# Optimization experiments

Hardware: AMD Instinct MI355X
Metric: run time of the kernel (lower is better)

The kernel has to match this reference:

```python
import jax, jax.numpy as jnp
import numpy as np
import math

CHUNK = 32
NS_STEPS = 5
MAX_GNORM = 10.0


def _normalize(x, eps=1e-12):
    n = jnp.linalg.norm(x, axis=-1, keepdims=True)
    return x / jnp.maximum(n, eps)


def _poly(x):  # poly_degree = 2: [x, x^2] / sqrt(2)
    return jnp.concatenate([x, x * x], axis=-1) / math.sqrt(2.0)


def _ns5(G):
    # Muon-style Newton-Schulz orthogonalization (quintic, 5 steps)
    a, b, c = 3.4445, -4.7750, 2.0315
    t = G.shape[0] > G.shape[1]
    X = G.T if t else G
    X = X / (jnp.linalg.norm(X) + 1e-7)
    for _ in range(NS_STEPS):
        A = X @ X.T
        B = b * A + c * (A @ A)
        X = a * X + B @ X
    return X.T if t else X


def _clip_mean(g):
    # per-sample grad-norm clipping to MAX_GNORM, then mean over samples
    n = g.shape[0]
    norms = jnp.maximum(jnp.linalg.norm(g.reshape(n, -1), axis=1), 1e-8)
    scale = jnp.maximum(norms / MAX_GNORM, 1.0)
    return jnp.mean(g / scale.reshape((n,) + (1,) * (g.ndim - 1)), axis=0)


def _mem_fwd(W0, W1, z):  # MemoryMLP depth=2, gelu (exact) between layers
    return jax.nn.gelu(z @ W0, approximate=False) @ W1


def setup_inputs() -> dict:
    key = jax.random.key(0)
    ks = jax.random.split(key, 16)
    B, S, D, M, P, H = 2, 1024, 2048, 512, 1024, 2048
    w = lambda k, shape, fan_in: jax.random.normal(k, shape, jnp.float32) / np.float32(np.sqrt(fan_in))
    return {
        "x": jax.random.normal(ks[0], (B, S, D), jnp.float32),
        "Wk": w(ks[1], (M, D), D),
        "Wv": w(ks[2], (M, D), D),
        "Wq": w(ks[3], (M, D), D),
        "Wout": w(ks[4], (D, M), M),
        "w_lr": w(ks[5], (1, D), D), "b_lr": jnp.full((1,), -4.0, jnp.float32),
        "w_mom": w(ks[6], (1, D), D), "b_mom": jnp.full((1,), 1.0, jnp.float32),
        "w_dec": w(ks[7], (1, D), D), "b_dec": jnp.full((1,), -3.0, jnp.float32),
        "w_gate": w(ks[8], (1, D), D), "b_gate": jnp.full((1,), -1.0, jnp.float32),
        "Wmem0": w(ks[9], (P, H), P),
        "Wmem1": w(ks[10], (H, P), H),
        "Wmemout": w(ks[11], (P, M), P),
        "Wvexp": w(ks[12], (M, P), M),
    }


def reference(x, Wk, Wv, Wq, Wout, w_lr, b_lr, w_mom, b_mom, w_dec, b_dec,
              w_gate, b_gate, Wmem0, Wmem1, Wmemout, Wvexp):
    # Inference path (torch.is_grad_enabled() == False): chunked ATLAS update.
    B, S, D = x.shape
    NC = S // CHUNK

    k = _normalize(x @ Wk.T)          # (B,S,M)
    v = x @ Wv.T                       # (B,S,M)
    q = _normalize(x @ Wq.T)          # (B,S,M)
    kp = _poly(k)                      # (B,S,P)
    qp = _poly(q)                      # (B,S,P)
    vexp = v @ Wvexp                   # v_expand: (B,S,P)

    gate = lambda w, b: jax.nn.sigmoid(jnp.einsum('bsd,od->bso', x, w) + b)
    lr, mom, dec, og = gate(w_lr, b_lr), gate(w_mom, b_mom), gate(w_dec, b_dec), gate(w_gate, b_gate)

    cmean = lambda t: t[..., 0].reshape(B, NC, CHUNK).mean(axis=(0, 2))  # per-chunk scalar
    lr_c, mom_c, dec_c = cmean(lr), cmean(mom), cmean(dec)

    chunks = lambda t: t.reshape(B, NC, CHUNK, t.shape[-1]).transpose(1, 0, 2, 3)  # (NC,B,C,F)
    qc, kc, vc = chunks(qp), chunks(kp), chunks(vexp)

    def loss_fn(params, kk, vv):  # ||M(k) - v||^2 per sample
        W0_, W1_ = params
        pred = jax.nn.gelu(kk @ W0_, approximate=False) @ W1_
        return jnp.sum((pred - vv) ** 2)

    grad_fn = jax.vmap(jax.grad(loss_fn), in_axes=((None, None), 0, 0))

    def step(carry, xs):
        W0, W1, S0, S1 = carry
        qch, kch, vch, lrc, momc, decc = xs
        retr = _mem_fwd(W0, W1, qch) @ Wmemout  # retrieve with pre-update params: (B,C,M)
        kf = kch.reshape(-1, kch.shape[-1])
        vf = vch.reshape(-1, vch.shape[-1])
        g0, g1 = grad_fn((W0, W1), kf, vf)      # per-sample grads
        g0, g1 = _clip_mean(g0), _clip_mean(g1)
        s0 = momc * S0 - lrc * g0                # surprise momentum
        s1 = momc * S1 - lrc * g1
        W0n = (1.0 - decc) * W0 + _ns5(s0) * lrc # forget gate + orthogonalized step
        W1n = (1.0 - decc) * W1 + _ns5(s1) * lrc
        return (W0n, W1n, s0, s1), retr

    init = (Wmem0, Wmem1, jnp.zeros_like(Wmem0), jnp.zeros_like(Wmem1))
    _, retrs = jax.lax.scan(step, init, (qc, kc, vc, lr_c, mom_c, dec_c))
    retrieved = retrs.transpose(1, 0, 2, 3).reshape(B, S, -1)  # (B,S,M)
    delta = retrieved @ Wout.T
    return x + delta * og
```

## Files before the change

### kernel.cpp

```cpp
#include <hip/hip_runtime.h>


typedef unsigned short us;
typedef __attribute__((ext_vector_type(8))) short s16x8;
typedef __attribute__((ext_vector_type(8))) unsigned short u16x8;
typedef __attribute__((ext_vector_type(4))) float f32x4;

#define MKP 72

__device__ __forceinline__ float gelu_f(float x) {
  return 0.5f * x * (1.0f + erff(x * 0.70710678118654752f));
}
__device__ __forceinline__ float gelu_grad_f(float x) {
  float cdf = 0.5f * (1.0f + erff(x * 0.70710678118654752f));
  float pdf = 0.3989422804014327f * expf(-0.5f * x * x);
  return cdf + x * pdf;
}
__device__ __forceinline__ float sigmoid_f(float x) { return 1.0f / (1.0f + expf(-x)); }

__device__ __forceinline__ us f2bf(float f) {
  union { float f; unsigned u; } v; v.f = f;
  unsigned r = (v.u + 0x7FFFu + ((v.u >> 16) & 1u)) >> 16;
  return (us)r;
}
__device__ __forceinline__ float bf2f(us h) {
  union { unsigned u; float f; } v; v.u = ((unsigned)h) << 16;
  return v.f;
}
__device__ __forceinline__ int cm_map(int n) {
  return ((n & 1023) >> 5) * 64 + (n >> 10) * 32 + (n & 31);
}
__device__ __forceinline__ size_t pf_off(int r, int k, int KB) {
  return ((size_t)(r >> 4) * KB + (k >> 5)) * 512 + ((k >> 3) & 3) * 128 + (r & 15) * 8 + (k & 7);
}

__device__ __forceinline__ float block_reduce_sum(float v, float* red) {
  int t = threadIdx.x;
  red[t] = v; __syncthreads();
  for (int s = blockDim.x >> 1; s > 0; s >>= 1) {
    if (t < s) red[t] += red[t + s];
    __syncthreads();
  }
  float r = red[0];
  __syncthreads();
  return r;
}

__device__ __forceinline__ void gemm_pk(const us* __restrict__ A,
                                        const us* __restrict__ B, int KB,
                                        int lane, int m0, int n0,
                                        f32x4 (&acc)[4][4]) {
  const us* am[4];
  const us* bm[4];
#pragma unroll
  for (int q = 0; q < 4; ++q) {
    am[q] = A + (size_t)((m0 >> 4) + q) * KB * 512 + lane * 8;
    bm[q] = B + (size_t)((n0 >> 4) + q) * KB * 512 + lane * 8;
  }
#pragma unroll
  for (int i = 0; i < 4; ++i)
#pragma unroll
    for (int j = 0; j < 4; ++j) acc[i][j] = (f32x4){0.f, 0.f, 0.f, 0.f};
  u16x8 a0[4], b0[4], a1[4], b1[4];
#pragma unroll
  for (int q = 0; q < 4; ++q) {
    a0[q] = *(const u16x8*)(am[q]);
    b0[q] = *(const u16x8*)(bm[q]);
    a1[q] = *(const u16x8*)(am[q] + 512);
    b1[q] = *(const u16x8*)(bm[q] + 512);
  }
  for (int kb = 0; kb < KB; kb += 2) {
#pragma unroll
    for (int mi = 0; mi < 4; ++mi)
#pragma unroll
      for (int ni = 0; ni < 4; ++ni)
        acc[mi][ni] = __builtin_amdgcn_mfma_f32_16x16x32_bf16(
            (s16x8)a0[mi], (s16x8)b0[ni], acc[mi][ni], 0, 0, 0);
    if (kb + 2 < KB) {
#pragma unroll
      for (int q = 0; q < 4; ++q) {
        a0[q] = *(const u16x8*)(am[q] + (size_t)(kb + 2) * 512);
        b0[q] = *(const u16x8*)(bm[q] + (size_t)(kb + 2) * 512);
      }
    }
#pragma unroll
    for (int mi = 0; mi < 4; ++mi)
#pragma unroll
      for (int ni = 0; ni < 4; ++ni)
        acc[mi][ni] = __builtin_amdgcn_mfma_f32_16x16x32_bf16(
            (s16x8)a1[mi], (s16x8)b1[ni], acc[mi][ni], 0, 0, 0);
    if (kb + 3 < KB) {
#pragma unroll
      for (int q = 0; q < 4; ++q) {
        a1[q] = *(const u16x8*)(am[q] + (size_t)(kb + 3) * 512);
        b1[q] = *(const u16x8*)(bm[q] + (size_t)(kb + 3) * 512);
      }
    }
  }
}

template<int EPI, int TM, int TN>
__global__ __launch_bounds__(256)
void mgp_k(const us* __restrict__ Aq, const us* __restrict__ Bq,
           us* __restrict__ Cq, us* __restrict__ C2q, const us* __restrict__ Eq,
           int K, int N, float c1, float c2,
           long sA, long sB, long sC, long sE) {
  __shared__ __align__(16) us ct[4 * 64 * 72];
  const int tid = threadIdx.x;
  const int wave = tid >> 6, lane = tid & 63;
  const int l15 = lane & 15, l4 = lane >> 4;
  const int wm = (wave >> 1) * 64, wn = (wave & 1) * 64;
  const int TPB = TM * TN;
  const int t = blockIdx.x;
  const int bz = t / TPB;
  const int ti = t - bz * TPB;
  const int m0 = (ti / TN) * 128 + wm;
  const int n0 = (ti % TN) * 128 + wn;

  const us* A = Aq + (size_t)bz * sA;
  const us* B = Bq + (size_t)bz * sB;
  us* C = Cq + (size_t)bz * sC;
  us* C2 = C2q + (size_t)bz * sC;
  const us* E = Eq + (size_t)bz * sE;
  const int KB = K >> 5;

  f32x4 acc[4][4];
  gemm_pk(A, B, KB, lane, m0, n0, acc);

  us* cw = ct + wave * 64 * 72;
#pragma unroll
  for (int mi = 0; mi < 4; ++mi)
#pragma unroll
    for (int i = 0; i < 4; ++i)
#pragma unroll
      for (int ni = 0; ni < 4; ++ni)
        cw[(mi * 16 + l4 * 4 + i) * 72 + ni * 16 + l15] = f2bf(acc[mi][ni][i]);

  if constexpr (EPI == 20 || EPI == 21) {
    const int KC = N >> 5;
#pragma unroll
    for (int q = 0; q < 8; ++q) {
      u16x8 v = *(const u16x8*)&cw[lane * 72 + q * 8];
      size_t off = pf_off(m0 + lane, n0 + q * 8, KC);
      if constexpr (EPI == 21) {
        u16x8 e = *(const u16x8*)(E + off);
        u16x8 o;
#pragma unroll
        for (int w = 0; w < 8; ++w) o[w] = f2bf(c1 * bf2f(v[w]) + c2 * bf2f(e[w]));
        *(u16x8*)(C + off) = o;
      } else {
        *(u16x8*)(C + off) = v;
      }
    }
  } else if constexpr (EPI == 23) {
#pragma unroll
    for (int q = 0; q < 8; ++q) {
      size_t off = pf_off(m0 + lane, n0 + q * 8, 64);
      u16x8 v = *(const u16x8*)&cw[lane * 72 + q * 8];
      u16x8 e = *(const u16x8*)(E + off);
      u16x8 o;
#pragma unroll
      for (int w = 0; w < 8; ++w) o[w] = f2bf(bf2f(v[w]) + c1 * bf2f(e[w]));
      *(u16x8*)&cw[lane * 72 + q * 8] = o;
      *(u16x8*)(C + off) = o;
    }
#pragma unroll
    for (int q = 0; q < 8; ++q) {
      u16x8 o;
#pragma unroll
      for (int w = 0; w < 8; ++w) o[w] = cw[(q * 8 + w) * 72 + lane];
      size_t offT = pf_off(n0 + lane, m0 + q * 8, 32);
      *(u16x8*)(C2 + offT) = o;
    }
  } else {
#pragma unroll
    for (int q = 0; q < 8; ++q) {
      size_t off = pf_off(m0 + lane, n0 + q * 8, 64);
      u16x8 v = *(const u16x8*)&cw[lane * 72 + q * 8];
      u16x8 e = *(const u16x8*)(E + off);
      u16x8 o;
#pragma unroll
      for (int w = 0; w < 8; ++w) o[w] = f2bf(bf2f(v[w]) + c1 * bf2f(e[w]));
      *(u16x8*)(C + (size_t)(m0 + lane) * 2048 + n0 + q * 8) = o;
    }
  }
}

template<int EPI, int TM, int TN>
static void mgp(hipStream_t st, const us* A, const us* B, us* C, us* C2,
                const us* E, int K, int N, float c1, float c2,
                long sA, long sB, long sC, long sE) {
  dim3 g(TM * TN * 2), b(256);
  hipLaunchKernelGGL((mgp_k<EPI, TM, TN>), g, b, 0, st, A, B, C, C2, E,
                     K, N, c1, c2, sA, sB, sC, sE);
}

template<int EPI>
__device__ __forceinline__ float epilogue(f32x4 (&acc)[4][4], int m0, int n0,
    int l15, int l4, void* Cq, void* C2, const void* Eq,
    const float* FX, const float* OG, const float* cp, int cidx,
    int ldc, int lde, float c1, float c2) {
  float ssq = 0.f;
#pragma unroll
  for (int mi = 0; mi < 4; ++mi) {
#pragma unroll
    for (int i = 0; i < 4; ++i) {
      int grow = m0 + mi * 16 + l4 * 4 + i;
#pragma unroll
      for (int ni = 0; ni < 4; ++ni) {
        int col = n0 + ni * 16 + l15;
        float v = acc[mi][ni][i];
        if constexpr (EPI == 5) {
          ((us*)Cq)[(size_t)grow * ldc + col] = f2bf(v);
        } else if constexpr (EPI == 7) {
          ((float*)Cq)[(size_t)grow * ldc + col] = v;
        } else if constexpr (EPI == 8) {
          ((us*)Cq)[(size_t)grow * ldc + col] = f2bf(gelu_f(v));
          if (m0 >= 64)
            ((float*)C2)[(size_t)(grow - 64) * ldc + col] = gelu_grad_f(v);
        } else if constexpr (EPI == 9) {
          if (m0 < 64)
            ((us*)Cq)[(size_t)grow * ldc + col] = f2bf(v);
          else
            ((us*)Cq)[(size_t)grow * ldc + col] =
                f2bf(2.0f * (v - ((const float*)Eq)[(size_t)(grow - 64) * lde + col]));
        } else if constexpr (EPI == 13) {
          ((float*)Cq)[(size_t)grow * ldc + col] =
              v * ((const float*)Eq)[(size_t)grow * lde + col];
        } else if constexpr (EPI == 14) {
          float* C = (float*)Cq;
          float old = C[(size_t)grow * ldc + col];
          float nv = cp[cidx * 3 + 1] * old - cp[cidx * 3 + 0] * v;
          C[(size_t)grow * ldc + col] = nv;
          ssq += nv * nv;
        } else if constexpr (EPI == 15) {
          ((float*)Cq)[(size_t)grow * ldc + col] =
              FX[(size_t)grow * ldc + col] + v * OG[grow];
        } else if constexpr (EPI == 17) {
          int crow = cm_map(grow);
          ((float*)Cq)[(size_t)crow * ldc + col] = v;
        }
      }
    }
  }
  return ssq;
}

template<int EPI, int TA, int DUAL, int AG>
__device__ __forceinline__ float mg_body(const us* __restrict__ A0,
    const us* __restrict__ A2, const us* __restrict__ B,
    void* __restrict__ Cq, void* __restrict__ C2, const void* __restrict__ Eq,
    const float* __restrict__ FX, const float* __restrict__ OG,
    const float* __restrict__ cp, int cidx, int m0, int n0,
    int K, int lda, int ldb, int ldc, int lde, float c1, float c2,
    us* As, us* Bs, int t) {
  const us* A = A0;
  if constexpr (DUAL) { if (m0 >= 64) A = A2; }
  const int mA0 = DUAL ? (m0 & 63) : m0;
  const int l15 = t & 15, l4 = t >> 4;

  f32x4 acc[4][4];
#pragma unroll
  for (int i = 0; i < 4; ++i)
#pragma unroll
    for (int j = 0; j < 4; ++j) acc[i][j] = (f32x4){0.f, 0.f, 0.f, 0.f};

  const int srw = t >> 3;
  const int sck = (t & 7) * 8;

  u16x8 ra[8], rb[8];
  auto LDA = [&](int k0) {
#pragma unroll
    for (int p = 0; p < 8; ++p) {
      if constexpr (TA == 0) {
        int row = srw + p * 8;
        int srow;
        if constexpr (AG) srow = cm_map(m0 + row); else srow = mA0 + row;
        ra[p] = *(const u16x8*)(A + (size_t)srow * lda + k0 + sck);
      } else {
        ra[p] = *(const u16x8*)(A + (size_t)(k0 + srw + p * 8) * lda + mA0 + sck);
      }
    }
  };
  auto LDB = [&](int k0) {
#pragma unroll
    for (int p = 0; p < 8; ++p)
      rb[p] = *(const u16x8*)(B + (size_t)(n0 + srw + p * 8) * ldb + k0 + sck);
  };

  LDA(0); LDB(0);
  for (int k0 = 0; k0 < K; k0 += 64) {
    if constexpr (TA == 0) {
#pragma unroll
      for (int p = 0; p < 8; ++p)
        *(u16x8*)&As[(srw + p * 8) * MKP + sck] = ra[p];
    } else {
#pragma unroll
      for (int p = 0; p < 8; ++p) {
        int kk = srw + p * 8;
#pragma unroll
        for (int j = 0; j < 8; ++j) As[(sck + j) * MKP + kk] = ra[p][j];
      }
    }
#pragma unroll
    for (int p = 0; p < 8; ++p)
      *(u16x8*)&Bs[(srw + p * 8) * MKP + sck] = rb[p];
    if (k0 + 64 < K) { LDA(k0 + 64); LDB(k0 + 64); }
#pragma unroll
    for (int ks = 0; ks < 2; ++ks) {
      s16x8 af[4], bf[4];
#pragma unroll
      for (int mi = 0; mi < 4; ++mi)
        af[mi] = *(const s16x8*)&As[(mi * 16 + l15) * MKP + ks * 32 + l4 * 8];
#pragma unroll
      for (int ni = 0; ni < 4; ++ni)
        bf[ni] = *(const s16x8*)&Bs[(ni * 16 + l15) * MKP + ks * 32 + l4 * 8];
#pragma unroll
      for (int mi = 0; mi < 4; ++mi)
#pragma unroll
        for (int ni = 0; ni < 4; ++ni)
          acc[mi][ni] = __builtin_amdgcn_mfma_f32_16x16x32_bf16(af[mi], bf[ni], acc[mi][ni], 0, 0, 0);
    }
  }

  return epilogue<EPI>(acc, m0, n0, l15, l4, Cq, C2, Eq, FX, OG, cp, cidx,
                       ldc, lde, c1, c2);
}

template<int EPI, int TA, int DUAL, int AG>
__global__ __launch_bounds__(64)
void mg_k(const us* __restrict__ Aq, const us* __restrict__ A2,
          const us* __restrict__ Bq, void* __restrict__ Cq,
          void* __restrict__ C2, const void* __restrict__ Eq,
          const float* __restrict__ FX, const float* __restrict__ OG,
          const float* __restrict__ cp, int cidx,
          int M, int N, int K, int lda, int ldb, int ldc, int lde,
          float c1, float c2) {
  __shared__ __align__(16) us As[64 * MKP];
  __shared__ __align__(16) us Bs[64 * MKP];
  mg_body<EPI, TA, DUAL, AG>(Aq, A2, Bq, Cq, C2, Eq, FX, OG, cp, cidx,
                             blockIdx.y * 64, blockIdx.x * 64, K, lda, ldb,
                             ldc, lde, c1, c2, As, Bs, threadIdx.x);
}

template<int EPI, int TA = 0, int DUAL = 0, int AG = 0>
static void mg(hipStream_t st, const us* A, const us* A2, const us* B,
               void* C, void* C2, const void* E,
               const float* FX, const float* OG, const float* cp, int cidx,
               int M, int N, int K, int lda, int ldb, int ldc, int lde,
               float c1 = 0.f, float c2 = 0.f) {
  dim3 g(N / 64, M / 64, 1), b(64);
  hipLaunchKernelGGL((mg_k<EPI, TA, DUAL, AG>), g, b, 0, st, A, A2, B, C, C2, E,
                     FX, OG, cp, cidx, M, N, K, lda, ldb, ldc, lde, c1, c2);
}

__global__ __launch_bounds__(64)
void mg2_k(const us* __restrict__ kp_c, const us* __restrict__ dhT,
           float* __restrict__ S0, const us* __restrict__ habk,
           const us* __restrict__ rbwT, float* __restrict__ S1,
           const float* __restrict__ cp, int c, float* __restrict__ parts2) {
  __shared__ __align__(16) us As[64 * MKP];
  __shared__ __align__(16) us Bs[64 * MKP];
  int bid = blockIdx.x;
  float ssq;
  if (bid < 512) {
    int m0 = (bid >> 5) * 64, n0 = (bid & 31) * 64;
    ssq = mg_body<14, 1, 0, 0>(kp_c, nullptr, dhT, S0, nullptr, nullptr,
                               nullptr, nullptr, cp, c, m0, n0,
                               64, 1024, 64, 2048, 0, 0.f, 0.f, As, Bs, threadIdx.x);
  } else {
    int b2 = bid - 512;
    int m0 = (b2 >> 4) * 64, n0 = (b2 & 15) * 64;
    ssq = mg_body<14, 1, 0, 0>(habk, nullptr, rbwT, S1, nullptr, nullptr,
                               nullptr, nullptr, cp, c, m0, n0,
                               64, 2048, 64, 1024, 0, 0.f, 0.f, As, Bs, threadIdx.x);
  }
  for (int off = 32; off > 0; off >>= 1) ssq += __shfl_down(ssq, off);
  if (threadIdx.x == 0) parts2[bid] = ssq;
}

__global__ __launch_bounds__(64)
void mg34_k(const us* __restrict__ pr, const us* __restrict__ WmoT,
            us* __restrict__ retrv_c, const us* __restrict__ W1b,
            float* __restrict__ dh, const float* __restrict__ gp) {
  __shared__ __align__(16) us As[64 * MKP];
  __shared__ __align__(16) us Bs[64 * MKP];
  int bid = blockIdx.x;
  if (bid < 8) {
    mg_body<5, 0, 0, 0>(pr, nullptr, WmoT, retrv_c, nullptr, nullptr,
                        nullptr, nullptr, nullptr, 0, 0, bid * 64,
                        1024, 1024, 1024, 512, 0, 0.f, 0.f, As, Bs, threadIdx.x);
  } else {
    int b2 = bid - 8;
    mg_body<13, 0, 0, 0>(pr + 64 * 1024, nullptr, W1b, dh, nullptr, gp,
                         nullptr, nullptr, nullptr, 0, 0, b2 * 64,
                         1024, 1024, 1024, 2048, 2048, 0.f, 0.f, As, Bs, threadIdx.x);
  }
}

__global__ void wt2_k(const float* __restrict__ dh, const float* __restrict__ w0inv,
                      us* __restrict__ dhT, const us* __restrict__ prg,
                      const float* __restrict__ w1inv, us* __restrict__ rbwT) {
  __shared__ float tile[32][33];
  int bid = blockIdx.x;
  int tx = threadIdx.x, ty = threadIdx.y;
  int c0, r0, ldin;
  const float* wv;
  us* outp;
  bool f32in;
  const void* in;
  if (bid < 128) {
    in = dh; wv = w0inv; outp = dhT; ldin = 2048; f32in = true;
    c0 = (bid & 63) * 32; r0 = (bid >> 6) * 32;
  } else {
    int b2 = bid - 128;
    in = prg; wv = w1inv; outp = rbwT; ldin = 1024; f32in = false;
    c0 = (b2 & 31) * 32; r0 = (b2 >> 5) * 32;
  }
#pragma unroll
  for (int j = 0; j < 4; ++j) {
    int r = r0 + ty + 8 * j, cc = c0 + tx;
    float v = f32in ? ((const float*)in)[(size_t)r * ldin + cc]
                    : bf2f(((const us*)in)[(size_t)r * ldin + cc]);
    tile[ty + 8 * j][tx] = v * wv[r];
  }
  __syncthreads();
#pragma unroll
  for (int j = 0; j < 4; ++j)
    outp[(size_t)(c0 + ty + 8 * j) * 64 + r0 + tx] = f2bf(tile[tx][ty + 8 * j]);
}

__global__ void scalepk2_k(const float* __restrict__ S0, const float* __restrict__ S1,
                           const float* __restrict__ inv01,
                           us* __restrict__ XP, us* __restrict__ XTP) {
  __shared__ float tile[32][33];
  const long SB2c = 2097152;
  int z = blockIdx.z;
  float s = inv01[z];
  int tx = threadIdx.x, ty = threadIdx.y;
  int r0, c0;
  const float* S;
  if (z == 0) { S = S0; c0 = blockIdx.x * 32; r0 = blockIdx.y * 32; }
  else        { S = S1; r0 = blockIdx.x * 32; c0 = blockIdx.y * 32; }
  int C = (z == 0) ? 2048 : 1024;
#pragma unroll
  for (int j = 0; j < 4; ++j)
    tile[ty + 8 * j][tx] = S[(size_t)(r0 + ty + 8 * j) * C + c0 + tx] * s;
  __syncthreads();
  us* xp = XP + (size_t)z * SB2c;
  us* xt = XTP + (size_t)z * SB2c;
  int t = ty * 32 + tx;
  if (t < 128) {
    int rh = t >> 2, cc = t & 3;
    u16x8 v;
#pragma unroll
    for (int e = 0; e < 8; ++e) v[e] = f2bf(tile[rh][cc * 8 + e]);
    if (z == 0) {
      *(u16x8*)(xp + pf_off(r0 + rh, c0 + cc * 8, 64)) = v;
    } else {
      *(u16x8*)(xt + pf_off(r0 + rh, c0 + cc * 8, 32)) = v;
    }
  } else {
    int ch = (t - 128) >> 2, rc = (t - 128) & 3;
    u16x8 v;
#pragma unroll
    for (int e = 0; e < 8; ++e) v[e] = f2bf(tile[rc * 8 + e][ch]);
    if (z == 0) {
      *(u16x8*)(xt + pf_off(c0 + ch, r0 + rc * 8, 32)) = v;
    } else {
      *(u16x8*)(xp + pf_off(c0 + ch, r0 + rc * 8, 64)) = v;
    }
  }
}


__global__ __launch_bounds__(256) void conv_k(const float* __restrict__ in,
                                              us* __restrict__ out, int n) {
  for (int i = blockIdx.x * 256 + threadIdx.x; i < n; i += gridDim.x * 256)
    out[i] = f2bf(in[i]);
}

__global__ void tconv_k(const float* __restrict__ in, us* __restrict__ out, int R, int C) {
  __shared__ float tile[32][33];
  int c0 = blockIdx.x * 32, r0 = blockIdx.y * 32;
  int tx = threadIdx.x, ty = threadIdx.y;
#pragma unroll
  for (int j = 0; j < 4; ++j)
    tile[ty + 8 * j][tx] = in[(size_t)(r0 + ty + 8 * j) * C + c0 + tx];
  __syncthreads();
#pragma unroll
  for (int j = 0; j < 4; ++j)
    out[(size_t)(c0 + ty + 8 * j) * R + r0 + tx] = f2bf(tile[tx][ty + 8 * j]);
}


__global__ __launch_bounds__(256) void polynorm2_k(const float* __restrict__ lin,
                                                   us* __restrict__ outp) {
  __shared__ float red[256];
  int n = blockIdx.x, t = threadIdx.x;
  int rowp = cm_map(n);
  float s = 0.f;
  for (int f = t; f < 512; f += 256) { float v = lin[(size_t)n * 512 + f]; s += v * v; }
  float tot = block_reduce_sum(s, red);
  float sc = 1.0f / fmaxf(sqrtf(tot), 1e-12f);
  const float is2 = 0.70710678118654752f;
  for (int f = t; f < 512; f += 256) {
    float v = lin[(size_t)n * 512 + f] * sc;
    outp[(size_t)rowp * 1024 + f] = f2bf(v * is2);
    outp[(size_t)rowp * 1024 + 512 + f] = f2bf(v * v * is2);
  }
}

__global__ __launch_bounds__(256) void gates_k(const float* __restrict__ x,
    const float* __restrict__ wlr, const float* __restrict__ blr,
    const float* __restrict__ wmom, const float* __restrict__ bmom,
    const float* __restrict__ wdec, const float* __restrict__ bdec,
    const float* __restrict__ wgate, const float* __restrict__ bgate,
    float* __restrict__ lrv, float* __restrict__ momv,
    float* __restrict__ decv, float* __restrict__ og) {
  __shared__ float red[256];
  int n = blockIdx.x, t = threadIdx.x;
  float s0 = 0.f, s1 = 0.f, s2 = 0.f, s3 = 0.f;
  for (int d = t; d < 2048; d += 256) {
    float xv = x[(size_t)n * 2048 + d];
    s0 += xv * wlr[d]; s1 += xv * wmom[d]; s2 += xv * wdec[d]; s3 += xv * wgate[d];
  }
  float r0 = block_reduce_sum(s0, red);
  float r1 = block_reduce_sum(s1, red);
  float r2 = block_reduce_sum(s2, red);
  float r3 = block_reduce_sum(s3, red);
  if (t == 0) {
    lrv[n] = sigmoid_f(r0 + blr[0]);
    momv[n] = sigmoid_f(r1 + bmom[0]);
    decv[n] = sigmoid_f(r2 + bdec[0]);
    og[n] = sigmoid_f(r3 + bgate[0]);
  }
}

__global__ void chunk_means_k(const float* __restrict__ lrv, const float* __restrict__ momv,
                              const float* __restrict__ decv, float* __restrict__ cp) {
  int c = blockIdx.x, t = threadIdx.x;
  int n = ((t >> 5) << 10) + c * 32 + (t & 31);
  float a = lrv[n], b = momv[n], d = decv[n];
  for (int off = 32; off > 0; off >>= 1) {
    a += __shfl_down(a, off);
    b += __shfl_down(b, off);
    d += __shfl_down(d, off);
  }
  if (t == 0) {
    cp[c * 3 + 0] = a * (1.f / 64.f);
    cp[c * 3 + 1] = b * (1.f / 64.f);
    cp[c * 3 + 2] = d * (1.f / 64.f);
  }
}

__global__ __launch_bounds__(256) void sampnorm2_k(const us* __restrict__ kp_b,
                                                   const float* __restrict__ dh,
                                                   const us* __restrict__ hab,
                                                   const us* __restrict__ pr,
                                                   float* __restrict__ w0inv,
                                                   float* __restrict__ w1inv, int c) {
  __shared__ float red[256];
  int i = blockIdx.x, t = threadIdx.x;
  int row = c * 64 + i;
  float sk = 0.f, sr = 0.f, sdh = 0.f, sa = 0.f;
  for (int p = t; p < 1024; p += 256) {
    float v = bf2f(kp_b[(size_t)row * 1024 + p]); sk += v * v;
    v = bf2f(pr[(size_t)(64 + i) * 1024 + p]); sr += v * v;
  }
  for (int h = t; h < 2048; h += 256) {
    float v = dh[(size_t)i * 2048 + h]; sdh += v * v;
    v = bf2f(hab[(size_t)(64 + i) * 2048 + h]); sa += v * v;
  }
  float tk = block_reduce_sum(sk, red);
  float tdh = block_reduce_sum(sdh, red);
  float ta = block_reduce_sum(sa, red);
  float tr = block_reduce_sum(sr, red);
  if (t == 0) {
    float n0 = fmaxf(sqrtf(tk) * sqrtf(tdh), 1e-8f);
    w0inv[i] = 1.0f / (64.0f * fmaxf(n0 * 0.1f, 1.0f));
    float n1 = fmaxf(sqrtf(ta) * sqrtf(tr), 1e-8f);
    w1inv[i] = 1.0f / (64.0f * fmaxf(n1 * 0.1f, 1.0f));
  }
}

__global__ __launch_bounds__(512) void frob_fin512_k(const float* __restrict__ parts2,
                                                     float* __restrict__ inv) {
  __shared__ float red[512];
  int z = blockIdx.x;
  float r = block_reduce_sum(parts2[z * 512 + threadIdx.x], red);
  if (threadIdx.x == 0) inv[z] = 1.0f / (sqrtf(r) + 1e-7f);
}

__global__ void wupd01_k(float* __restrict__ W0, const us* __restrict__ X0,
                         us* __restrict__ W0bT,
                         float* __restrict__ W1, const us* __restrict__ X2,
                         us* __restrict__ W1b, us* __restrict__ W1bT,
                         const float* __restrict__ cp, int c) {
  __shared__ float tA[32][33];
  __shared__ float tB[32][33];
  float lr = cp[c * 3 + 0], om = 1.0f - cp[c * 3 + 2];
  int tx = threadIdx.x, ty = threadIdx.y;
  if (blockIdx.z == 0) {
    int c0 = blockIdx.x * 32, r0 = blockIdx.y * 32;
#pragma unroll
    for (int j = 0; j < 4; ++j) {
      int r = r0 + ty + 8 * j, h = c0 + tx;
      size_t idx = (size_t)r * 2048 + h;
      float v = om * W0[idx] + lr * bf2f(X0[idx]);
      W0[idx] = v;
      tA[ty + 8 * j][tx] = v;
    }
    __syncthreads();
#pragma unroll
    for (int j = 0; j < 4; ++j)
      W0bT[(size_t)(c0 + ty + 8 * j) * 1024 + r0 + tx] = f2bf(tA[tx][ty + 8 * j]);
  } else {
    int h0 = blockIdx.x * 32, p0 = blockIdx.y * 32;
#pragma unroll
    for (int j = 0; j < 4; ++j)
      tA[ty + 8 * j][tx] = bf2f(X2[(size_t)(p0 + ty + 8 * j) * 2048 + h0 + tx]);
    __syncthreads();
#pragma unroll
    for (int j = 0; j < 4; ++j) {
      int h = h0 + ty + 8 * j, p = p0 + tx;
      size_t idx = (size_t)h * 1024 + p;
      float v = om * W1[idx] + lr * tA[tx][ty + 8 * j];
      W1[idx] = v;
      W1b[idx] = f2bf(v);
      tB[tx][ty + 8 * j] = v;
    }
    __syncthreads();
#pragma unroll
    for (int j = 0; j < 4; ++j)
      W1bT[(size_t)(p0 + ty + 8 * j) * 2048 + h0 + tx] = f2bf(tB[ty + 8 * j][tx]);
  }
}


extern "C" void kernel_launch(void* const* d_in, const int* in_sizes, int n_in,
                              void* d_out, int out_size, void* d_ws, size_t ws_size,
                              hipStream_t stream) {
  const float* x = (const float*)d_in[0];
  const float* Wk = (const float*)d_in[1];
  const float* Wv = (const float*)d_in[2];
  const float* Wq = (const float*)d_in[3];
  const float* Wout = (const float*)d_in[4];
  const float* w_lr = (const float*)d_in[5];
  const float* b_lr = (const float*)d_in[6];
  const float* w_mom = (const float*)d_in[7];
  const float* b_mom = (const float*)d_in[8];
  const float* w_dec = (const float*)d_in[9];
  const float* b_dec = (const float*)d_in[10];
  const float* w_gate = (const float*)d_in[11];
  const float* b_gate = (const float*)d_in[12];
  const float* Wmem0 = (const float*)d_in[13];
  const float* Wmem1 = (const float*)d_in[14];
  const float* Wmemout = (const float*)d_in[15];
  const float* Wvexp = (const float*)d_in[16];
  float* out = (float*)d_out;
  (void)n_in; (void)in_sizes; (void)out_size;

  const long F = 1048576;
  const long BIG = 2097152;
  const long SB2 = 2097152, SB1 = 1048576;
  float* ws = (float*)d_ws;
  if (ws_size < (size_t)25043464 * sizeof(float)) return;

  us* kp_b   = (us*)ws;
  us* qp_b   = (us*)(ws + F);
  float* vexp = ws + 2 * F;
  float* W0  = ws + 4 * F;
  float* W1  = ws + 6 * F;
  float* S0  = ws + 8 * F;
  float* S1  = ws + 10 * F;
  us* XPong  = (us*)(ws + 12 * F);
  us* XTPong = (us*)(ws + 14 * F);
  us* XPing  = (us*)(ws + 16 * F);
  us* AP     = (us*)(ws + 18 * F);
  float* SCR = ws + 19 * F;
  us* XTPing = (us*)(ws + 20 * F);
  us* BP     = (us*)(ws + 22 * F);
  us* W0bT   = (us*)(ws + 20 * F);
  us* W1bT   = (us*)(ws + 21 * F);
  us* W1b    = (us*)(ws + 22 * F);
  us* WmoT   = (us*)(ws + 23 * F);
  us* retrv  = (us*)(ws + 23 * F + 262144);
  float* smal = ws + 23 * F + 262144 + 524288;
  float* og   = smal;
  float* lrv  = og + 2048;
  float* momv = lrv + 2048;
  float* decv = momv + 2048;
  float* cpb  = decv + 2048;
  float* w0inv = cpb + 128;
  float* w1inv = w0inv + 64;
  float* parts2 = w1inv + 64;
  float* inv01 = parts2 + 1024;

  us* xb   = XPong;
  us* Wkb  = XTPong;
  us* Wqb  = XTPong + 1048576;
  us* Wvb  = XTPong + 2097152;
  us* vlin = XPing;
  us* WvexpT = XPing + 1048576;
  us* Woutb = AP;
  float* lin = SCR;
  us* hab   = (us*)SCR;
  float* gp = SCR + 131072;
  us* pr    = (us*)(SCR + 262144);
  float* dh = SCR + 327680;
  us* dhT   = (us*)(SCR + 458752);
  us* rbwT  = (us*)(SCR + 524288);
  us* Xfin  = XPong;

  const float NSa = 3.4445f, NSb = -4.7750f, NSc = 2.0315f;

  hipMemcpyAsync(W0, Wmem0, (size_t)BIG * 4, hipMemcpyDeviceToDevice, stream);
  hipMemcpyAsync(W1, Wmem1, (size_t)BIG * 4, hipMemcpyDeviceToDevice, stream);
  hipMemsetAsync(S0, 0, (size_t)BIG * 4, stream);
  hipMemsetAsync(S1, 0, (size_t)BIG * 4, stream);
  hipLaunchKernelGGL(tconv_k, dim3(64, 32), dim3(32, 8), 0, stream, Wmem0, W0bT, 1024, 2048);
  hipLaunchKernelGGL(conv_k, dim3(1024), dim3(256), 0, stream, Wmem1, W1b, (int)BIG);
  hipLaunchKernelGGL(tconv_k, dim3(32, 64), dim3(32, 8), 0, stream, Wmem1, W1bT, 2048, 1024);
  hipLaunchKernelGGL(tconv_k, dim3(16, 32), dim3(32, 8), 0, stream, Wmemout, WmoT, 1024, 512);
  hipLaunchKernelGGL(tconv_k, dim3(32, 16), dim3(32, 8), 0, stream, Wvexp, WvexpT, 512, 1024);
  hipLaunchKernelGGL(conv_k, dim3(2048), dim3(256), 0, stream, x, xb, 2048 * 2048);
  hipLaunchKernelGGL(conv_k, dim3(512), dim3(256), 0, stream, Wk, Wkb, 512 * 2048);
  hipLaunchKernelGGL(conv_k, dim3(512), dim3(256), 0, stream, Wq, Wqb, 512 * 2048);
  hipLaunchKernelGGL(conv_k, dim3(512), dim3(256), 0, stream, Wv, Wvb, 512 * 2048);

  mg<7>(stream, xb, nullptr, Wkb, lin, nullptr, nullptr, nullptr, nullptr, nullptr, 0,
        2048, 512, 2048, 2048, 2048, 512, 0);
  hipLaunchKernelGGL(polynorm2_k, dim3(2048), dim3(256), 0, stream, lin, kp_b);
  mg<7>(stream, xb, nullptr, Wqb, lin, nullptr, nullptr, nullptr, nullptr, nullptr, 0,
        2048, 512, 2048, 2048, 2048, 512, 0);
  hipLaunchKernelGGL(polynorm2_k, dim3(2048), dim3(256), 0, stream, lin, qp_b);
  mg<5>(stream, xb, nullptr, Wvb, vlin, nullptr, nullptr, nullptr, nullptr, nullptr, 0,
        2048, 512, 2048, 2048, 2048, 512, 0);
  mg<17>(stream, vlin, nullptr, WvexpT, vexp, nullptr, nullptr, nullptr, nullptr, nullptr, 0,
         2048, 1024, 512, 512, 512, 1024, 0);

  hipLaunchKernelGGL(gates_k, dim3(2048), dim3(256), 0, stream, x,
                     w_lr, b_lr, w_mom, b_mom, w_dec, b_dec, w_gate, b_gate,
                     lrv, momv, decv, og);
  hipLaunchKernelGGL(chunk_means_k, dim3(32), dim3(64), 0, stream, lrv, momv, decv, cpb);

  for (int c = 0; c < 32; ++c) {
    const us* kp_c = kp_b + (size_t)c * 64 * 1024;
    const us* qp_c = qp_b + (size_t)c * 64 * 1024;
    const float* vexp_c = vexp + (size_t)c * 64 * 1024;
    mg<8, 0, 1>(stream, qp_c, kp_c, W0bT, hab, gp, nullptr, nullptr, nullptr, nullptr, 0,
                128, 2048, 1024, 1024, 1024, 2048, 0);
    mg<9>(stream, hab, nullptr, W1bT, pr, nullptr, vexp_c, nullptr, nullptr, nullptr, 0,
          128, 1024, 2048, 2048, 2048, 1024, 1024);
    hipLaunchKernelGGL(mg34_k, dim3(40), dim3(64), 0, stream,
                       pr, WmoT, retrv + (size_t)c * 64 * 512, W1b, dh, gp);
    hipLaunchKernelGGL(sampnorm2_k, dim3(64), dim3(256), 0, stream,
                       kp_b, dh, hab, pr, w0inv, w1inv, c);
    hipLaunchKernelGGL(wt2_k, dim3(192), dim3(32, 8), 0, stream,
                       dh, w0inv, dhT, pr + 64 * 1024, w1inv, rbwT);
    hipLaunchKernelGGL(mg2_k, dim3(1024), dim3(64), 0, stream,
                       kp_c, dhT, S0, hab + 64 * 2048, rbwT, S1, cpb, c, parts2);
    hipLaunchKernelGGL(frob_fin512_k, dim3(2), dim3(512), 0, stream, parts2, inv01);
    hipLaunchKernelGGL(scalepk2_k, dim3(64, 32, 2), dim3(32, 8), 0, stream,
                       S0, S1, inv01, XPing, XTPing);

    us* xpA[2] = {XPing, XPong};
    us* xtA[2] = {XTPing, XTPong};
    int cur = 0;
    for (int it = 0; it < 5; ++it) {
      const us* XPc = xpA[cur];
      const us* XTPc = xtA[cur];
      int nxt = cur ^ 1;
      mgp<20, 8, 8>(stream, XPc, XPc, AP, nullptr, nullptr, 2048, 1024,
                    0.f, 0.f, SB2, SB2, SB1, 0);
      mgp<21, 8, 8>(stream, AP, AP, BP, nullptr, AP, 1024, 1024,
                    NSc, NSb, SB1, SB1, SB1, SB1);
      if (it < 4) {
        mgp<23, 8, 16>(stream, BP, XTPc, xpA[nxt], xtA[nxt], XPc, 1024, 2048,
                       NSa, 0.f, SB1, SB2, SB2, SB2);
        cur = nxt;
      } else {
        mgp<24, 8, 16>(stream, BP, XTPc, Xfin, nullptr, XPc, 1024, 2048,
                       NSa, 0.f, SB1, SB2, SB2, SB2);
      }
    }
    hipLaunchKernelGGL(wupd01_k, dim3(64, 32, 2), dim3(32, 8), 0, stream,
                       W0, Xfin, W0bT, W1, Xfin + SB2, W1b, W1bT, cpb, c);
  }

  hipLaunchKernelGGL(conv_k, dim3(1024), dim3(256), 0, stream, Wout, Woutb, 2048 * 512);
  mg<15, 0, 0, 1>(stream, retrv, nullptr, Woutb, out, nullptr, nullptr, x, og, nullptr, 0,
                  2048, 2048, 512, 512, 512, 2048, 0);
}
```

Before: 14.31 ms.

## Fuse weight update into final Newton-Schulz GEMM and fold norm finalize into scaling

The last Newton-Schulz iteration now applies the decayed weight update directly in its epilogue, writing W0/W0bT and W1/W1b/W1bT and dropping the separate wupd01 kernel and the Xfin round trip. The Frobenius-norm finalization kernel is removed, and each scalepk2 block now reduces the 512 partial sums itself. This saves two launches per chunk plus some global traffic. In exchange the reduction is repeated in every block, and the W1 path in the fused epilogue uses strided scalar global accesses.

```diff
diff --git a/kernel.cpp b/kernel.cpp
--- a/kernel.cpp
+++ b/kernel.cpp
@@ -38,6 +38,17 @@
   int t = threadIdx.x;
   red[t] = v; __syncthreads();
   for (int s = blockDim.x >> 1; s > 0; s >>= 1) {
+    if (t < s) red[t] += red[t + s];
+    __syncthreads();
+  }
+  float r = red[0];
+  __syncthreads();
+  return r;
+}
+
+__device__ __forceinline__ float block_reduce_sum256(float v, float* red, int t) {
+  red[t] = v; __syncthreads();
+  for (int s = 128; s > 0; s >>= 1) {
     if (t < s) red[t] += red[t + s];
     __syncthreads();
   }
@@ -172,17 +183,6 @@
       size_t offT = pf_off(n0 + lane, m0 + q * 8, 32);
       *(u16x8*)(C2 + offT) = o;
     }
-  } else {
-#pragma unroll
-    for (int q = 0; q < 8; ++q) {
-      size_t off = pf_off(m0 + lane, n0 + q * 8, 64);
-      u16x8 v = *(const u16x8*)&cw[lane * 72 + q * 8];
-      u16x8 e = *(const u16x8*)(E + off);
-      u16x8 o;
-#pragma unroll
-      for (int w = 0; w < 8; ++w) o[w] = f2bf(bf2f(v[w]) + c1 * bf2f(e[w]));
-      *(u16x8*)(C + (size_t)(m0 + lane) * 2048 + n0 + q * 8) = o;
-    }
   }
 }
 
@@ -193,6 +193,91 @@
   dim3 g(TM * TN * 2), b(256);
   hipLaunchKernelGGL((mgp_k<EPI, TM, TN>), g, b, 0, st, A, B, C, C2, E,
                      K, N, c1, c2, sA, sB, sC, sE);
+}
+
+__global__ __launch_bounds__(256)
+void mgpW_k(const us* __restrict__ BP, const us* __restrict__ XTPc,
+            const us* __restrict__ XPc,
+            float* __restrict__ W0, us* __restrict__ W0bT,
+            float* __restrict__ W1, us* __restrict__ W1b, us* __restrict__ W1bT,
+            const float* __restrict__ cp, int cidx, float nsa,
+            long sA, long sB, long sE) {
+  __shared__ __align__(16) us ct[4 * 64 * 72];
+  const int tid = threadIdx.x;
+  const int wave = tid >> 6, lane = tid & 63;
+  const int l15 = lane & 15, l4 = lane >> 4;
+  const int wm = (wave >> 1) * 64, wn = (wave & 1) * 64;
+  const int TPB = 8 * 16;
+  const int t = blockIdx.x;
+  const int bz = t / TPB;
+  const int ti = t - bz * TPB;
+  const int m0 = (ti / 16) * 128 + wm;
+  const int n0 = (ti % 16) * 128 + wn;
+
+  const us* A = BP + (size_t)bz * sA;
+  const us* B = XTPc + (size_t)bz * sB;
+  const us* E = XPc + (size_t)bz * sE;
+  const float lr = cp[cidx * 3 + 0], om = 1.0f - cp[cidx * 3 + 2];
+
+  f32x4 acc[4][4];
+  gemm_pk(A, B, 32, lane, m0, n0, acc);
+
+  us* cw = ct + wave * 64 * 72;
+#pragma unroll
+  for (int mi = 0; mi < 4; ++mi)
+#pragma unroll
+    for (int i = 0; i < 4; ++i)
+#pragma unroll
+      for (int ni = 0; ni < 4; ++ni)
+        cw[(mi * 16 + l4 * 4 + i) * 72 + ni * 16 + l15] = f2bf(acc[mi][ni][i]);
+
+#pragma unroll
+  for (int q = 0; q < 8; ++q) {
+    size_t off = pf_off(m0 + lane, n0 + q * 8, 64);
+    u16x8 v = *(const u16x8*)&cw[lane * 72 + q * 8];
+    u16x8 e = *(const u16x8*)(E + off);
+    u16x8 o;
+#pragma unroll
+    for (int w = 0; w < 8; ++w) o[w] = f2bf(bf2f(v[w]) + nsa * bf2f(e[w]));
+    *(u16x8*)&cw[lane * 72 + q * 8] = o;
+  }
+
+  if (bz == 0) {
+#pragma unroll
+    for (int q = 0; q < 8; ++q) {
+      size_t idx = (size_t)(m0 + lane) * 2048 + n0 + q * 8;
+#pragma unroll
+      for (int w = 0; w < 8; ++w) {
+        float x = bf2f(cw[lane * 72 + q * 8 + w]);
+        float nv = om * W0[idx + w] + lr * x;
+        W0[idx + w] = nv;
+        cw[lane * 72 + q * 8 + w] = f2bf(nv);
+      }
+    }
+#pragma unroll
+    for (int q = 0; q < 8; ++q) {
+      u16x8 o;
+#pragma unroll
+      for (int w = 0; w < 8; ++w) o[w] = cw[(q * 8 + w) * 72 + lane];
+      *(u16x8*)&W0bT[(size_t)(n0 + lane) * 1024 + m0 + q * 8] = o;
+    }
+  } else {
+    for (int h = 0; h < 64; ++h) {
+      size_t idx = (size_t)(n0 + h) * 1024 + m0 + lane;
+      float x = bf2f(cw[lane * 72 + h]);
+      float nv = om * W1[idx] + lr * x;
+      W1[idx] = nv;
+      W1b[idx] = f2bf(nv);
+      cw[lane * 72 + h] = f2bf(nv);
+    }
+#pragma unroll
+    for (int q = 0; q < 8; ++q) {
+      u16x8 o;
+#pragma unroll
+      for (int w = 0; w < 8; ++w) o[w] = cw[lane * 72 + q * 8 + w];
+      *(u16x8*)&W1bT[(size_t)(m0 + lane) * 2048 + n0 + q * 8] = o;
+    }
+  }
 }
 
 template<int EPI>
@@ -431,13 +516,18 @@
 }
 
 __global__ void scalepk2_k(const float* __restrict__ S0, const float* __restrict__ S1,
-                           const float* __restrict__ inv01,
+                           const float* __restrict__ parts2,
                            us* __restrict__ XP, us* __restrict__ XTP) {
   __shared__ float tile[32][33];
+  __shared__ float red[256];
   const long SB2c = 2097152;
   int z = blockIdx.z;
-  float s = inv01[z];
   int tx = threadIdx.x, ty = threadIdx.y;
+  int t = ty * 32 + tx;
+  float p = parts2[z * 512 + t] + parts2[z * 512 + 256 + t];
+  float tot = block_reduce_sum256(p, red, t);
+  float s = 1.0f / (sqrtf(tot) + 1e-7f);
+
   int r0, c0;
   const float* S;
   if (z == 0) { S = S0; c0 = blockIdx.x * 32; r0 = blockIdx.y * 32; }
@@ -449,7 +539,6 @@
   __syncthreads();
   us* xp = XP + (size_t)z * SB2c;
   us* xt = XTP + (size_t)z * SB2c;
-  int t = ty * 32 + tx;
   if (t < 128) {
     int rh = t >> 2, cc = t & 3;
     u16x8 v;
@@ -581,59 +670,6 @@
     w0inv[i] = 1.0f / (64.0f * fmaxf(n0 * 0.1f, 1.0f));
     float n1 = fmaxf(sqrtf(ta) * sqrtf(tr), 1e-8f);
     w1inv[i] = 1.0f / (64.0f * fmaxf(n1 * 0.1f, 1.0f));
-  }
-}
-
-__global__ __launch_bounds__(512) void frob_fin512_k(const float* __restrict__ parts2,
-                                                     float* __restrict__ inv) {
-  __shared__ float red[512];
-  int z = blockIdx.x;
-  float r = block_reduce_sum(parts2[z * 512 + threadIdx.x], red);
-  if (threadIdx.x == 0) inv[z] = 1.0f / (sqrtf(r) + 1e-7f);
-}
-
-__global__ void wupd01_k(float* __restrict__ W0, const us* __restrict__ X0,
-                         us* __restrict__ W0bT,
-                         float* __restrict__ W1, const us* __restrict__ X2,
-                         us* __restrict__ W1b, us* __restrict__ W1bT,
-                         const float* __restrict__ cp, int c) {
-  __shared__ float tA[32][33];
-  __shared__ float tB[32][33];
-  float lr = cp[c * 3 + 0], om = 1.0f - cp[c * 3 + 2];
-  int tx = threadIdx.x, ty = threadIdx.y;
-  if (blockIdx.z == 0) {
-    int c0 = blockIdx.x * 32, r0 = blockIdx.y * 32;
-#pragma unroll
-    for (int j = 0; j < 4; ++j) {
-      int r = r0 + ty + 8 * j, h = c0 + tx;
-      size_t idx = (size_t)r * 2048 + h;
-      float v = om * W0[idx] + lr * bf2f(X0[idx]);
-      W0[idx] = v;
-      tA[ty + 8 * j][tx] = v;
-    }
-    __syncthreads();
-#pragma unroll
-    for (int j = 0; j < 4; ++j)
-      W0bT[(size_t)(c0 + ty + 8 * j) * 1024 + r0 + tx] = f2bf(tA[tx][ty + 8 * j]);
-  } else {
-    int h0 = blockIdx.x * 32, p0 = blockIdx.y * 32;
-#pragma unroll
-    for (int j = 0; j < 4; ++j)
-      tA[ty + 8 * j][tx] = bf2f(X2[(size_t)(p0 + ty + 8 * j) * 2048 + h0 + tx]);
-    __syncthreads();
-#pragma unroll
-    for (int j = 0; j < 4; ++j) {
-      int h = h0 + ty + 8 * j, p = p0 + tx;
-      size_t idx = (size_t)h * 1024 + p;
-      float v = om * W1[idx] + lr * tA[tx][ty + 8 * j];
-      W1[idx] = v;
-      W1b[idx] = f2bf(v);
-      tB[tx][ty + 8 * j] = v;
-    }
-    __syncthreads();
-#pragma unroll
-    for (int j = 0; j < 4; ++j)
-      W1bT[(size_t)(p0 + ty + 8 * j) * 2048 + h0 + tx] = f2bf(tB[ty + 8 * j][tx]);
   }
 }
 
@@ -695,7 +731,6 @@
   float* w0inv = cpb + 128;
   float* w1inv = w0inv + 64;
   float* parts2 = w1inv + 64;
-  float* inv01 = parts2 + 1024;
 
   us* xb   = XPong;
   us* Wkb  = XTPong;
@@ -711,7 +746,6 @@
   float* dh = SCR + 327680;
   us* dhT   = (us*)(SCR + 458752);
   us* rbwT  = (us*)(SCR + 524288);
-  us* Xfin  = XPong;
 
   const float NSa = 3.4445f, NSb = -4.7750f, NSc = 2.0315f;
 
@@ -761,9 +795,8 @@
                        dh, w0inv, dhT, pr + 64 * 1024, w1inv, rbwT);
     hipLaunchKernelGGL(mg2_k, dim3(1024), dim3(64), 0, stream,
                        kp_c, dhT, S0, hab + 64 * 2048, rbwT, S1, cpb, c, parts2);
-    hipLaunchKernelGGL(frob_fin512_k, dim3(2), dim3(512), 0, stream, parts2, inv01);
     hipLaunchKernelGGL(scalepk2_k, dim3(64, 32, 2), dim3(32, 8), 0, stream,
-                       S0, S1, inv01, XPing, XTPing);
+                       S0, S1, parts2, XPing, XTPing);
 
     us* xpA[2] = {XPing, XPong};
     us* xtA[2] = {XTPing, XTPong};
@@ -781,12 +814,11 @@
                        NSa, 0.f, SB1, SB2, SB2, SB2);
         cur = nxt;
       } else {
-        mgp<24, 8, 16>(stream, BP, XTPc, Xfin, nullptr, XPc, 1024, 2048,
-                       NSa, 0.f, SB1, SB2, SB2, SB2);
+        hipLaunchKernelGGL(mgpW_k, dim3(256), dim3(256), 0, stream,
+                           BP, XTPc, XPc, W0, W0bT, W1, W1b, W1bT,
+                           cpb, c, NSa, SB1, SB2, SB2);
       }
     }
-    hipLaunchKernelGGL(wupd01_k, dim3(64, 32, 2), dim3(32, 8), 0, stream,
-                       W0, Xfin, W0bT, W1, Xfin + SB2, W1b, W1bT, cpb, c);
   }
 
   hipLaunchKernelGGL(conv_k, dim3(1024), dim3(256), 0, stream, Wout, Woutb, 2048 * 512);
```

Result: no change. 14.42 ms (+0.8%).
